# Kernel optimization log

Hardware: AMD Instinct MI355X
Metric: run time of the kernel (lower is better)

The kernel has to match this reference:

```python
import jax, jax.numpy as jnp
import numpy as np

B, L, DM = 4, 2048, 1024  # batch, seq len (== l_max, global kernel), d_model; head_dim = 1


def setup_inputs() -> dict:
    key = jax.random.key(0)
    ks = jax.random.split(key, 13)
    n = lambda k, shape, s=1.0: jax.random.normal(k, shape, dtype=jnp.float32) * s
    W_SCALE = 0.02   # keeps activations well-conditioned through the chained convs
    K_SCALE = 0.02
    return {
        "u": n(ks[0], (B, L, DM)),
        "Wq": n(ks[1], (DM, DM), W_SCALE), "bq": n(ks[2], (DM,), W_SCALE),
        "Wk": n(ks[3], (DM, DM), W_SCALE), "bk": n(ks[4], (DM,), W_SCALE),
        "Wv": n(ks[5], (DM, DM), W_SCALE), "bv": n(ks[6], (DM,), W_SCALE),
        "k_kernel": n(ks[7], (DM, L), K_SCALE),
        "k_D": n(ks[8], (DM,)),
        "ssm_kernel": n(ks[9], (DM, L), K_SCALE),
        "D": n(ks[10], (DM,)),
        "Wo": n(ks[11], (DM, DM), W_SCALE), "bo": n(ks[12], (DM,), W_SCALE),
    }


def reference(u, Wq, bq, Wk, bk, Wv, bv, k_kernel, k_D, ssm_kernel, D, Wo, bo):
    # u: (B, L, H) with H = d_model (head_dim = 1)
    Lseq = u.shape[1]
    fft_size = 2 * Lseq  # zero-pad to 2L for linear (causal) convolution

    # q/k/v projections -> (B, H, L)
    q = jnp.einsum('blh,dh->bdl', u, Wq) + bq[None, :, None]
    k = jnp.einsum('blh,dh->bdl', u, Wk) + bk[None, :, None]
    v = jnp.einsum('blh,dh->bdl', u, Wv) + bv[None, :, None]

    # shift conv on k: k <- k_kernel * k (causal FFT conv) + k_D * k
    k_kernel_f = jnp.fft.rfft(k_kernel, n=fft_size)           # (H, F)
    k_f = jnp.fft.rfft(k, n=fft_size)                          # (B, H, F)
    shift_k = jnp.fft.irfft(k_kernel_f[None] * k_f, n=fft_size)[..., :Lseq]
    k = shift_k + k_D[None, :, None] * k

    # head_dim == 1: kv outer product collapses to elementwise gate
    kv = k * v                                                 # (B, H, L)

    # ssm conv on kv (torch's 1/fft_size + norm='forward' irfft == standard irfft)
    kv_f = jnp.fft.rfft(kv, n=fft_size)                        # (B, H, F)
    ssm_kernel_f = jnp.fft.rfft(ssm_kernel, n=fft_size)        # (H, F)
    y = jnp.fft.irfft(kv_f * ssm_kernel_f[None], n=fft_size)[..., :Lseq]
    y = y + kv * D[None, :, None]                              # D skip

    # q gating, then output projection
    y = y * q                                                  # (B, H, L)
    y = jnp.swapaxes(y, 1, 2)                                  # (B, L, H)
    return jnp.einsum('blh,oh->blo', y, Wo) + bo
```

## Files before the change

kernel.cpp:

```cpp
#include <hip/hip_runtime.h>
#include <hip/hip_bf16.h>
#include <stdint.h>

#define DM   1024
#define LSEQ 2048
#define NB   4

typedef __attribute__((ext_vector_type(8))) short  short8;
typedef __attribute__((ext_vector_type(4))) float  floatx4;

__device__ __forceinline__ ushort f2b(float x) {
    union { float f; uint32_t u; } v; v.f = x;
    uint32_t b = v.u + 0x7FFF + ((v.u >> 16) & 1);
    return (ushort)(b >> 16);
}
__device__ __forceinline__ float b2f(ushort x) {
    union { uint32_t u; float f; } v; v.u = ((uint32_t)x) << 16;
    return v.f;
}

__global__ __launch_bounds__(256) void cvt_all_kernel(const float* __restrict__ u,
                                                      const float* __restrict__ Wq,
                                                      const float* __restrict__ Wk,
                                                      const float* __restrict__ Wv,
                                                      const float* __restrict__ Wo,
                                                      ushort* __restrict__ U16,
                                                      ushort* __restrict__ Wcat) {
    const int nu  = NB * LSEQ * DM / 8;
    const int per = DM * DM / 8;
    int i = blockIdx.x * 256 + threadIdx.x;
    const float* src; ushort* dst; int j;
    if (i < nu) { src = u; dst = U16; j = i; }
    else {
        int k = i - nu;
        int r = k / per;
        src = (r == 0) ? Wq : (r == 1) ? Wk : (r == 2) ? Wv : Wo;
        dst = Wcat + (size_t)r * (DM * DM);
        j = k - r * per;
    }
    const float4* p = (const float4*)src + (size_t)j * 2;
    float4 a = p[0], b = p[1];
    union { ushort us[8]; uint4 v; } o;
    o.us[0] = f2b(a.x); o.us[1] = f2b(a.y); o.us[2] = f2b(a.z); o.us[3] = f2b(a.w);
    o.us[4] = f2b(b.x); o.us[5] = f2b(b.y); o.us[6] = f2b(b.z); o.us[7] = f2b(b.w);
    *(uint4*)(dst + (size_t)j * 8) = o.v;
}

template <int MODE>
__global__ __launch_bounds__(512, 2) void gemm_8p(const ushort* __restrict__ Aw,
                                                  const ushort* __restrict__ Bw,
                                                  const float* __restrict__ b0,
                                                  const float* __restrict__ b1,
                                                  const float* __restrict__ b2,
                                                  void* __restrict__ C0v,
                                                  void* __restrict__ C1v,
                                                  void* __restrict__ C2v,
                                                  int N, int nbx) {
    constexpr int K = 1024, BK = 64, NT = K / BK;
    __shared__ char lds[131072];

    const int tid   = threadIdx.x;
    const int wave  = tid >> 6;
    const int lane  = tid & 63;
    const int qlane = lane & 15;
    const int qk    = lane >> 4;
    const int z7    = qlane & 7;
    const int wm    = wave >> 2;
    const int wn    = wave & 3;

    int flat = blockIdx.y * nbx + blockIdx.x;
    int nwg  = nbx * gridDim.y;
    int swz  = (flat & 7) * (nwg >> 3) + (flat >> 3);
    const int tn = (swz % nbx) * 256;
    const int tm = (swz / nbx) * 256;

    const int srcChunkOff   = (((lane & 7) ^ (lane >> 3)) * 8);
    const int srcRowInSlice = (lane >> 3);

#define STAGE_H(TT, ISB, H)                                                                   \
    {                                                                                         \
        const ushort* gbase = (ISB) ? Bw : Aw;                                                \
        const int trow = ((ISB) ? tn : tm) + (H) * 128 + wave * 16 + srcRowInSlice;           \
        char* dst = lds + ((ISB) ? 65536 : 0) + ((((TT) & 1) * 2 + (H)) * 16384) + wave * 2048; \
        const int k0_ = (TT) * BK;                                                            \
        _Pragma("unroll")                                                                     \
        for (int j = 0; j < 2; ++j) {                                                         \
            const ushort* src = gbase + (size_t)(trow + j * 8) * K + k0_ + srcChunkOff;       \
            __builtin_amdgcn_global_load_lds(                                                 \
                (const __attribute__((address_space(1))) void*)src,                           \
                (__attribute__((address_space(3))) void*)(dst + j * 1024), 16, 0, 0);         \
        }                                                                                     \
    }

    short8 af[4][2], af2[4][2], bf0[2][2], bf1[2][2];
    floatx4 acc[2][2][4][2] = {};

#define LDA(TT, MH, AF)                                                                       \
    {                                                                                         \
        const char* Ab = lds + ((((TT) & 1) * 2 + (MH)) * 16384);                             \
        _Pragma("unroll")                                                                     \
        for (int i = 0; i < 4; ++i) {                                                         \
            int lr = wm * 64 + i * 16 + qlane;                                                \
            _Pragma("unroll")                                                                 \
            for (int ks = 0; ks < 2; ++ks)                                                    \
                AF[i][ks] = *(const short8*)(Ab + lr * 128 + (((ks * 4 + qk) ^ z7) << 4));    \
        }                                                                                     \
    }
#define LDB(TT, NH, BF)                                                                       \
    {                                                                                         \
        const char* Bb = lds + 65536 + ((((TT) & 1) * 2 + (NH)) * 16384);                     \
        _Pragma("unroll")                                                                     \
        for (int j = 0; j < 2; ++j) {                                                         \
            int lr = wn * 32 + j * 16 + qlane;                                                \
            _Pragma("unroll")                                                                 \
            for (int ks = 0; ks < 2; ++ks)                                                    \
                BF[j][ks] = *(const short8*)(Bb + lr * 128 + (((ks * 4 + qk) ^ z7) << 4));    \
        }                                                                                     \
    }
#define MFMAQ(MH, NH, AF, BF)                                                                 \
    __builtin_amdgcn_s_setprio(1);                                                           \
    _Pragma("unroll")                                                                         \
    for (int ks = 0; ks < 2; ++ks)                                                            \
        _Pragma("unroll")                                                                     \
        for (int i = 0; i < 4; ++i)                                                           \
            _Pragma("unroll")                                                                 \
            for (int j = 0; j < 2; ++j)                                                       \
                acc[MH][NH][i][j] = __builtin_amdgcn_mfma_f32_16x16x32_bf16(                  \
                    AF[i][ks], BF[j][ks], acc[MH][NH][i][j], 0, 0, 0);                        \
    __builtin_amdgcn_s_setprio(0);
#define BARX  __builtin_amdgcn_s_barrier(); __builtin_amdgcn_sched_barrier(0)

    STAGE_H(0, 0, 0); STAGE_H(0, 1, 0); STAGE_H(0, 1, 1); STAGE_H(0, 0, 1);
    STAGE_H(1, 0, 0); STAGE_H(1, 1, 0); STAGE_H(1, 1, 1);
    asm volatile("s_waitcnt vmcnt(6)" ::: "memory");
    BARX;
    LDA(0, 0, af); LDB(0, 0, bf0);

    for (int t = 0; t < NT; ++t) {
        if (t + 1 < NT) STAGE_H(t + 1, 0, 1);
        LDB(t, 1, bf1);
        MFMAQ(0, 0, af, bf0);
        BARX;
        if (t + 2 < NT) STAGE_H(t + 2, 0, 0);
        LDA(t, 1, af2);
        MFMAQ(0, 1, af, bf1);
        BARX;
        if (t + 2 < NT) STAGE_H(t + 2, 1, 0);
        MFMAQ(1, 0, af2, bf0);
        BARX;
        if (t + 2 < NT) STAGE_H(t + 2, 1, 1);
        if (t + 2 < NT)      { asm volatile("s_waitcnt vmcnt(6)" ::: "memory"); }
        else if (t + 1 < NT) { asm volatile("s_waitcnt vmcnt(0)" ::: "memory"); }
        BARX;
        if (t + 1 < NT) { LDA(t + 1, 0, af); LDB(t + 1, 0, bf0); }
        MFMAQ(1, 1, af2, bf1);
    }
#undef STAGE_H
#undef LDA
#undef LDB
#undef MFMAQ
#undef BARX

#pragma unroll
    for (int mh = 0; mh < 2; ++mh)
#pragma unroll
    for (int nh = 0; nh < 2; ++nh)
#pragma unroll
    for (int i = 0; i < 4; ++i)
#pragma unroll
    for (int j = 0; j < 2; ++j) {
        int n  = tn + nh * 128 + wn * 32 + j * 16 + qlane;
        int m0 = tm + mh * 128 + wm * 64 + i * 16 + qk * 4;
        if (MODE == 0) {
            int proj = n >> 10, dd = n & (DM - 1);
            const float* bb = (proj == 0) ? b0 : (proj == 1) ? b1 : b2;
            ushort* Cb      = (ushort*)((proj == 0) ? C0v : (proj == 1) ? C1v : C2v);
            float bv = bb[dd];
            int b = m0 >> 11, l = m0 & (LSEQ - 1);
            ushort4 val;
            val.x = f2b(acc[mh][nh][i][j][0] + bv);
            val.y = f2b(acc[mh][nh][i][j][1] + bv);
            val.z = f2b(acc[mh][nh][i][j][2] + bv);
            val.w = f2b(acc[mh][nh][i][j][3] + bv);
            *(ushort4*)(Cb + ((size_t)b * DM + dd) * LSEQ + l) = val;
        } else {
            float* C0 = (float*)C0v;
            float bv = b0[n];
#pragma unroll
            for (int r = 0; r < 4; ++r)
                C0[(size_t)(m0 + r) * N + n] = acc[mh][nh][i][j][r] + bv;
        }
    }
}

template <int MODE>
__global__ __launch_bounds__(512, 2) void gemm_bt2(const ushort* __restrict__ Aw,
                                                   const ushort* __restrict__ Bw,
                                                   const float* __restrict__ b0,
                                                   const float* __restrict__ b1,
                                                   const float* __restrict__ b2,
                                                   void* __restrict__ C0v,
                                                   void* __restrict__ C1v,
                                                   void* __restrict__ C2v,
                                                   int M, int N, int K, int nbx) {
    constexpr int BM = 128, BN = 256, BK = 64;
    constexpr int BUFB = 49152;
    __shared__ char lds[3 * BUFB];

    const int tid   = threadIdx.x;
    const int wave  = tid >> 6;
    const int lane  = tid & 63;
    const int qlane = lane & 15;
    const int qk    = lane >> 4;

    int flat = blockIdx.y * nbx + blockIdx.x;
    int nwg  = nbx * gridDim.y;
    int swz  = (flat & 7) * (nwg >> 3) + (flat >> 3);
    const int tn = (swz % nbx) * BN;
    const int tm = (swz / nbx) * BM;

    const int wmo = (wave >> 2) * 64;
    const int wno = (wave & 3) * 64;
    const int NT  = K / BK;

#define STAGE(kt, p)                                                                          \
    {                                                                                         \
        const int k0_ = (kt) * BK;                                                            \
        char* Ab_ = lds + (p) * BUFB;                                                         \
        char* Bb_ = Ab_ + 16384;                                                              \
        _Pragma("unroll")                                                                     \
        for (int j = 0; j < 2; ++j) {                                                         \
            int id = wave * 64 + lane + j * 512;                                              \
            int row = id >> 3, s = id & 7;                                                    \
            const ushort* src = Aw + (size_t)(tm + row) * K + k0_ + ((s ^ (row & 7)) * 8);    \
            __builtin_amdgcn_global_load_lds((const __attribute__((address_space(1))) void*)src, \
                (__attribute__((address_space(3))) void*)(Ab_ + wave * 1024 + j * 8192), 16, 0, 0); \
        }                                                                                     \
        _Pragma("unroll")                                                                     \
        for (int j = 0; j < 4; ++j) {                                                         \
            int id = wave * 64 + lane + j * 512;                                              \
            int row = id >> 3, s = id & 7;                                                    \
            const ushort* src = Bw + (size_t)(tn + row) * K + k0_ + ((s ^ (row & 7)) * 8);    \
            __builtin_amdgcn_global_load_lds((const __attribute__((address_space(1))) void*)src, \
                (__attribute__((address_space(3))) void*)(Bb_ + wave * 1024 + j * 8192), 16, 0, 0); \
        }                                                                                     \
    }

    floatx4 acc[4][4] = {};

    STAGE(0, 0);
    STAGE(1, 1);

    const int z7 = qlane & 7;

    for (int t = 0; t < NT; ++t) {
        const int cur = t % 3;
        if (t < NT - 1) asm volatile("s_waitcnt vmcnt(6)" ::: "memory");
        else            asm volatile("s_waitcnt vmcnt(0)" ::: "memory");
        __builtin_amdgcn_s_barrier();
        __builtin_amdgcn_sched_barrier(0);

        if (t + 2 < NT) STAGE(t + 2, (t + 2) % 3);

        const char* Ab = lds + cur * BUFB;
        const char* Bb = Ab + 16384;
#pragma unroll
        for (int kk = 0; kk < 2; ++kk) {
            const int slot = ((kk * 4 + qk) ^ z7) << 4;
            short8 af[4], bfv[4];
#pragma unroll
            for (int i = 0; i < 4; ++i) {
                int r = wmo + i * 16 + qlane;
                af[i] = *(const short8*)(Ab + r * 128 + slot);
            }
#pragma unroll
            for (int j = 0; j < 4; ++j) {
                int r = wno + j * 16 + qlane;
                bfv[j] = *(const short8*)(Bb + r * 128 + slot);
            }
            __builtin_amdgcn_s_setprio(1);
#pragma unroll
            for (int i = 0; i < 4; ++i)
#pragma unroll
                for (int j = 0; j < 4; ++j)
                    acc[i][j] = __builtin_amdgcn_mfma_f32_16x16x32_bf16(af[i], bfv[j], acc[i][j], 0, 0, 0);
            __builtin_amdgcn_s_setprio(0);
        }
    }
#undef STAGE

#pragma unroll
    for (int i = 0; i < 4; ++i) {
#pragma unroll
        for (int j = 0; j < 4; ++j) {
            int n  = tn + wno + j * 16 + qlane;
            int m0 = tm + wmo + i * 16 + qk * 4;
            if (MODE == 0) {
                int proj = n >> 10, dd = n & (DM - 1);
                const float* bb = (proj == 0) ? b0 : (proj == 1) ? b1 : b2;
                ushort* Cb      = (ushort*)((proj == 0) ? C0v : (proj == 1) ? C1v : C2v);
                float bv = bb[dd];
                int b = m0 >> 11, l = m0 & (LSEQ - 1);
                ushort4 val;
                val.x = f2b(acc[i][j][0] + bv);
                val.y = f2b(acc[i][j][1] + bv);
                val.z = f2b(acc[i][j][2] + bv);
                val.w = f2b(acc[i][j][3] + bv);
                *(ushort4*)(Cb + ((size_t)b * DM + dd) * LSEQ + l) = val;
            } else {
                float* C0 = (float*)C0v;
                float bv = b0[n];
#pragma unroll
                for (int r = 0; r < 4; ++r)
                    C0[(size_t)(m0 + r) * N + n] = acc[i][j][r] + bv;
            }
        }
    }
}

#define KSTR 2096
#define XSTR 2248

__global__ __launch_bounds__(512) void conv_fused_kernel(const ushort* __restrict__ x,
                                                         const float* __restrict__ ker1,
                                                         const float* __restrict__ scale1,
                                                         const ushort* __restrict__ gate1,
                                                         const float* __restrict__ ker2,
                                                         const float* __restrict__ scale2,
                                                         const ushort* __restrict__ gate2,
                                                         ushort* __restrict__ out) {
    __shared__ ushort krev1[KSTR];
    __shared__ ushort krev2[KSTR];
    __shared__ ushort xs[4 * XSTR];
    const int d    = blockIdx.x;
    const int tid  = threadIdx.x;
    const int wave = tid >> 6;
    const int lane = tid & 63;

    {
        int b = wave >> 1, half = wave & 1;
        const ushort* src = x + ((size_t)b * DM + d) * LSEQ + half * 1024 + lane * 8;
        char* dst = (char*)xs + b * (XSTR * 2) + 256 + half * 2048;
#pragma unroll
        for (int c = 0; c < 2; ++c)
            __builtin_amdgcn_global_load_lds((const __attribute__((address_space(1))) void*)(src + c * 512),
                                             (__attribute__((address_space(3))) void*)(dst + c * 1024),
                                             16, 0, 0);
    }
    {
        int e0 = tid * 4;
        float4 k1 = *(const float4*)(ker1 + (size_t)d * LSEQ + e0);
        float4 k2 = *(const float4*)(ker2 + (size_t)d * LSEQ + e0);
        ushort4 o1, o2;
        o1.x = f2b(k1.w); o1.y = f2b(k1.z); o1.z = f2b(k1.y); o1.w = f2b(k1.x);
        o2.x = f2b(k2.w); o2.y = f2b(k2.z); o2.z = f2b(k2.y); o2.w = f2b(k2.x);
        *(ushort4*)(krev1 + (2060 - e0)) = o1;
        *(ushort4*)(krev2 + (2060 - e0)) = o2;
        uint4 z = {0, 0, 0, 0};
        if (tid < 2) {
            *(uint4*)((char*)krev1 + tid * 16) = z;
            *(uint4*)((char*)krev2 + tid * 16) = z;
        }
        if (tid >= 2 && tid < 6) {
            *(uint4*)((char*)krev1 + 4128 + (tid - 2) * 16) = z;
            *(uint4*)((char*)krev2 + 4128 + (tid - 2) * 16) = z;
        }
        if (tid >= 64 && tid < 128) {
            int b = (tid - 64) >> 4, c = (tid - 64) & 15;
            *(uint4*)((char*)xs + b * (XSTR * 2) + c * 16) = z;
        }
        if (tid >= 128 && tid < 144) {
            int b = (tid - 128) >> 2, c = (tid - 128) & 3;
            *(uint4*)((char*)xs + b * (XSTR * 2) + 4352 + c * 16) = z;
        }
    }
    __syncthreads();

    const int qn = lane & 15;
    const int qk = lane >> 4;

    int g[2] = {wave, 15 - wave};
    const int smax_all = 128 * (15 - wave) + 128;

    const int lbase = (qn & 3) * XSTR + 128 + 16 * (qn >> 2) + 8 * qk;

#define CSTEP(KR, ACC, SS, FP)                                                               \
    {                                                                                        \
        int b_el = 2063 - qn + 8 * qk - (SS);                                                \
        int A0 = b_el & ~3;                                                                  \
        uint2 w0 = *(const uint2*)((KR) + A0);                                               \
        uint2 w1 = *(const uint2*)((KR) + A0 + 4);                                           \
        uint2 w2 = *(const uint2*)((KR) + A0 + 8);                                           \
        int qsel = (b_el >> 1) & 1;                                                          \
        uint sh  = (uint)(b_el & 1) * 16u;                                                   \
        uint e0 = qsel ? w0.y : w0.x;                                                        \
        uint e1 = qsel ? w1.x : w0.y;                                                        \
        uint e2 = qsel ? w1.y : w1.x;                                                        \
        uint e3 = qsel ? w2.x : w1.y;                                                        \
        uint e4 = qsel ? w2.y : w2.x;                                                        \
        union { uint u[4]; short8 v; } Af;                                                   \
        Af.u[0] = __builtin_amdgcn_alignbit(e1, e0, sh);                                     \
        Af.u[1] = __builtin_amdgcn_alignbit(e2, e1, sh);                                     \
        Af.u[2] = __builtin_amdgcn_alignbit(e3, e2, sh);                                     \
        Af.u[3] = __builtin_amdgcn_alignbit(e4, e3, sh);                                     \
        _Pragma("unroll")                                                                    \
        for (int gi = 0; gi < 2; ++gi) {                                                     \
            if ((SS) <= 128 * g[gi] + 128) {                                                 \
                short8 fN = *(const short8*)(xs + lbase + 128 * g[gi] - (SS));               \
                ACC[gi][0] = __builtin_amdgcn_mfma_f32_16x16x32_bf16(Af.v, fN, ACC[gi][0], 0, 0, 0); \
                ACC[gi][1] = __builtin_amdgcn_mfma_f32_16x16x32_bf16(Af.v, FP[gi], ACC[gi][1], 0, 0, 0); \
                FP[gi] = fN;                                                                 \
            }                                                                                \
        }                                                                                    \
    }

    {
        floatx4 acc[2][2] = {};
        short8 fE[2], fO[2];
#pragma unroll
        for (int gi = 0; gi < 2; ++gi) {
            fE[gi] = *(const short8*)(xs + lbase + 128 * g[gi] + 64);
            fO[gi] = *(const short8*)(xs + lbase + 128 * g[gi] + 32);
        }
        for (int s = 0; s <= smax_all; s += 64) {
            CSTEP(krev1, acc, s, fE);
            if (s + 32 <= smax_all) CSTEP(krev1, acc, s + 32, fO);
        }

        __syncthreads();
        const float sc = scale1[d];
#pragma unroll
        for (int gi = 0; gi < 2; ++gi) {
#pragma unroll
            for (int m = 0; m < 2; ++m) {
                int p  = 8 * g[gi] + 4 * m + (qn >> 2);
                int b  = qn & 3;
                int l0 = 16 * p + 4 * qk;
                size_t off = ((size_t)b * DM + d) * LSEQ + l0;
                ushort4 xv = *(const ushort4*)(xs + b * XSTR + 128 + l0);
                ushort4 gv = *(const ushort4*)(gate1 + off);
                ushort4 ov;
                ov.x = f2b((acc[gi][m][0] + sc * b2f(xv.x)) * b2f(gv.x));
                ov.y = f2b((acc[gi][m][1] + sc * b2f(xv.y)) * b2f(gv.y));
                ov.z = f2b((acc[gi][m][2] + sc * b2f(xv.z)) * b2f(gv.z));
                ov.w = f2b((acc[gi][m][3] + sc * b2f(xv.w)) * b2f(gv.w));
                *(ushort4*)(xs + b * XSTR + 128 + l0) = ov;
            }
        }
        __syncthreads();
    }

    {
        floatx4 acc[2][2] = {};
        short8 fE[2], fO[2];
#pragma unroll
        for (int gi = 0; gi < 2; ++gi) {
            fE[gi] = *(const short8*)(xs + lbase + 128 * g[gi] + 64);
            fO[gi] = *(const short8*)(xs + lbase + 128 * g[gi] + 32);
        }
        for (int s = 0; s <= smax_all; s += 64) {
            CSTEP(krev2, acc, s, fE);
            if (s + 32 <= smax_all) CSTEP(krev2, acc, s + 32, fO);
        }

        const float sc = scale2[d];
#pragma unroll
        for (int gi = 0; gi < 2; ++gi) {
#pragma unroll
            for (int m = 0; m < 2; ++m) {
                int p  = 8 * g[gi] + 4 * m + (qn >> 2);
                int b  = qn & 3;
                int l0 = 16 * p + 4 * qk;
                size_t off = ((size_t)b * DM + d) * LSEQ + l0;
                ushort4 xv = *(const ushort4*)(xs + b * XSTR + 128 + l0);
                ushort4 gv = *(const ushort4*)(gate2 + off);
                ushort4 ov;
                ov.x = f2b((acc[gi][m][0] + sc * b2f(xv.x)) * b2f(gv.x));
                ov.y = f2b((acc[gi][m][1] + sc * b2f(xv.y)) * b2f(gv.y));
                ov.z = f2b((acc[gi][m][2] + sc * b2f(xv.z)) * b2f(gv.z));
                ov.w = f2b((acc[gi][m][3] + sc * b2f(xv.w)) * b2f(gv.w));
                *(ushort4*)(out + off) = ov;
            }
        }
    }
#undef CSTEP
}

__global__ __launch_bounds__(256) void transpose_bf16(const ushort* __restrict__ in,
                                                      ushort* __restrict__ out) {
    __shared__ ushort t[32][36];
    const int l0 = blockIdx.x * 32;
    const int d0 = blockIdx.y * 32;
    const int b  = blockIdx.z;
    const int q  = threadIdx.x & 7;
    const int r  = threadIdx.x >> 3;
    *(ushort4*)(&t[r][q * 4]) = *(const ushort4*)(in + ((size_t)b * DM + d0 + r) * LSEQ + l0 + q * 4);
    __syncthreads();
    ushort4 o;
    o.x = t[q * 4 + 0][r]; o.y = t[q * 4 + 1][r]; o.z = t[q * 4 + 2][r]; o.w = t[q * 4 + 3][r];
    *(ushort4*)(out + ((size_t)b * LSEQ + l0 + r) * DM + d0 + q * 4) = o;
}

extern "C" void kernel_launch(void* const* d_in, const int* in_sizes, int n_in,
                              void* d_out, int out_size, void* d_ws, size_t ws_size,
                              hipStream_t stream) {
    const float* u        = (const float*)d_in[0];
    const float* Wq       = (const float*)d_in[1];
    const float* bq       = (const float*)d_in[2];
    const float* Wk       = (const float*)d_in[3];
    const float* bk       = (const float*)d_in[4];
    const float* Wv       = (const float*)d_in[5];
    const float* bv       = (const float*)d_in[6];
    const float* k_kernel = (const float*)d_in[7];
    const float* k_D      = (const float*)d_in[8];
    const float* ssm_ker  = (const float*)d_in[9];
    const float* Dv       = (const float*)d_in[10];
    const float* Wo       = (const float*)d_in[11];
    const float* bo       = (const float*)d_in[12];
    float* outp = (float*)d_out;

    char* ws = (char*)d_ws;
    ushort* Q    = (ushort*)(ws);
    ushort* KV   = (ushort*)(ws + (16ull << 20));
    ushort* V    = (ushort*)(ws + (32ull << 20));
    ushort* U16  = (ushort*)(ws + (48ull << 20));
    ushort* YT   = (ushort*)(ws + (64ull << 20));
    ushort* Wcat = (ushort*)(ws + (80ull << 20));

    const int nu = NB * LSEQ * DM / 8, nw = 4 * DM * DM / 8;
    cvt_all_kernel<<<(nu + nw) / 256, 256, 0, stream>>>(u, Wq, Wk, Wv, Wo, U16, Wcat);

    dim3 g1(3 * DM / 256, NB * LSEQ / 256);
    gemm_8p<0><<<g1, 512, 0, stream>>>(U16, Wcat, bq, bk, bv, Q, KV, V,
                                       3 * DM, 3 * DM / 256);

    conv_fused_kernel<<<DM, 512, 0, stream>>>(KV, k_kernel, k_D, V, ssm_ker, Dv, Q, KV);

    dim3 g2(LSEQ / 32, DM / 32, NB);
    transpose_bf16<<<g2, 256, 0, stream>>>(KV, YT);

    dim3 g3(DM / 256, NB * LSEQ / 128);
    gemm_bt2<1><<<g3, 512, 0, stream>>>(YT, Wcat + 3 * DM * DM, bo, bo, bo,
                                        outp, outp, outp, NB * LSEQ, DM, DM, DM / 256);
}
```

Measured before the change: 162.6 us.

## Unify GEMMs into templated 128xBN ping-pong kernel with 384-wide QKV tiles

Replaces the 256x256 QKV GEMM and the separate triple-buffered output GEMM with one templated kernel using 128-row tiles and a configurable N width (384 for QKV, 256 for output). The pipeline stages whole A/B k-tiles two steps ahead with double buffering and alternates A fragment registers across unrolled tile pairs. The QKV grid changes from 12x32 to 8x64 workgroups, which alters wave balance across CUs and per-tile reuse. The output GEMM loses its three-stage buffer in favour of two stages. A leftover dead STAGE_B macro definition is left in the source.

```diff
diff --git a/kernel.cpp b/kernel.cpp
--- a/kernel.cpp
+++ b/kernel.cpp
@@ -46,8 +46,8 @@
     *(uint4*)(dst + (size_t)j * 8) = o.v;
 }
 
-template <int MODE>
-__global__ __launch_bounds__(512, 2) void gemm_8p(const ushort* __restrict__ Aw,
+template <int MODE, int BN>
+__global__ __launch_bounds__(512, 2) void gemm_v2(const ushort* __restrict__ Aw,
                                                   const ushort* __restrict__ Bw,
                                                   const float* __restrict__ b0,
                                                   const float* __restrict__ b1,
@@ -57,7 +57,12 @@
                                                   void* __restrict__ C2v,
                                                   int N, int nbx) {
     constexpr int K = 1024, BK = 64, NT = K / BK;
-    __shared__ char lds[131072];
+    constexpr int BM     = 128;
+    constexpr int NJH    = BN / 128;
+    constexpr int ASLOT  = BM * 128;
+    constexpr int BSLOT  = BN * 128;
+    constexpr int BOFF   = 2 * ASLOT;
+    __shared__ char lds[BOFF + 2 * BSLOT];
 
     const int tid   = threadIdx.x;
     const int wave  = tid >> 6;
@@ -71,33 +76,59 @@
     int flat = blockIdx.y * nbx + blockIdx.x;
     int nwg  = nbx * gridDim.y;
     int swz  = (flat & 7) * (nwg >> 3) + (flat >> 3);
-    const int tn = (swz % nbx) * 256;
-    const int tm = (swz / nbx) * 256;
-
-    const int srcChunkOff   = (((lane & 7) ^ (lane >> 3)) * 8);
-    const int srcRowInSlice = (lane >> 3);
-
-#define STAGE_H(TT, ISB, H)                                                                   \
-    {                                                                                         \
-        const ushort* gbase = (ISB) ? Bw : Aw;                                                \
-        const int trow = ((ISB) ? tn : tm) + (H) * 128 + wave * 16 + srcRowInSlice;           \
-        char* dst = lds + ((ISB) ? 65536 : 0) + ((((TT) & 1) * 2 + (H)) * 16384) + wave * 2048; \
+    const int tn = (swz % nbx) * BN;
+    const int tm = (swz / nbx) * BM;
+
+    const int srcChunkOff = ((lane & 7) ^ (lane >> 3)) * 8;
+    const int srcRow      = lane >> 3;
+
+#define STAGE_A(TT)                                                                           \
+    {                                                                                         \
+        const int trow = tm + wave * 16 + srcRow;                                             \
+        char* dst = lds + ((TT) & 1) * ASLOT + wave * 2048;                                   \
         const int k0_ = (TT) * BK;                                                            \
         _Pragma("unroll")                                                                     \
         for (int j = 0; j < 2; ++j) {                                                         \
-            const ushort* src = gbase + (size_t)(trow + j * 8) * K + k0_ + srcChunkOff;       \
+            const ushort* src = Aw + (size_t)(trow + j * 8) * K + k0_ + srcChunkOff;          \
             __builtin_amdgcn_global_load_lds(                                                 \
                 (const __attribute__((address_space(1))) void*)src,                           \
                 (__attribute__((address_space(3))) void*)(dst + j * 1024), 16, 0, 0);         \
         }                                                                                     \
     }
-
-    short8 af[4][2], af2[4][2], bf0[2][2], bf1[2][2];
-    floatx4 acc[2][2][4][2] = {};
-
-#define LDA(TT, MH, AF)                                                                       \
-    {                                                                                         \
-        const char* Ab = lds + ((((TT) & 1) * 2 + (MH)) * 16384);                             \
+#define STAGE_B(TT, H)                                                                        \
+    {                                                                                         \
+        const int rbase = (H) * (BN / 2) + wave * (8 * NJH);                                  \
+        const int trow  = tn + rbase + srcRow;                                                \
+        char* dst = lds + BOFF + ((TT) & 1) * BSLOT + rbase * 128;                            \
+        const int k0_ = (TT) * BK;                                                            \
+        _Pragma("unroll")                                                                     \
+        for (int j = 0; j < NJH; ++j) {                                                       \
+            const ushort* src = Bw + (size_t)(trow + j * 8) * K + k0_ + srcChunkOff;          \
+            __builtin_amdgcn_global_lds(0);                                                   \
+        }                                                                                     \
+    }
+#undef STAGE_B
+#define STAGE_B(TT, H)                                                                        \
+    {                                                                                         \
+        const int rbase = (H) * (BN / 2) + wave * (8 * NJH);                                  \
+        const int trow  = tn + rbase + srcRow;                                                \
+        char* dst = lds + BOFF + ((TT) & 1) * BSLOT + rbase * 128;                            \
+        const int k0_ = (TT) * BK;                                                            \
+        _Pragma("unroll")                                                                     \
+        for (int j = 0; j < NJH; ++j) {                                                       \
+            const ushort* src = Bw + (size_t)(trow + j * 8) * K + k0_ + srcChunkOff;          \
+            __builtin_amdgcn_global_load_lds(                                                 \
+                (const __attribute__((address_space(1))) void*)src,                           \
+                (__attribute__((address_space(3))) void*)(dst + j * 1024), 16, 0, 0);         \
+        }                                                                                     \
+    }
+
+    short8 afA[4][2], afB[4][2], bf0[NJH][2], bf1[NJH][2];
+    floatx4 acc[2][4][NJH] = {};
+
+#define LDA(TT, AF)                                                                           \
+    {                                                                                         \
+        const char* Ab = lds + ((TT) & 1) * ASLOT;                                            \
         _Pragma("unroll")                                                                     \
         for (int i = 0; i < 4; ++i) {                                                         \
             int lr = wm * 64 + i * 16 + qlane;                                                \
@@ -108,69 +139,74 @@
     }
 #define LDB(TT, NH, BF)                                                                       \
     {                                                                                         \
-        const char* Bb = lds + 65536 + ((((TT) & 1) * 2 + (NH)) * 16384);                     \
-        _Pragma("unroll")                                                                     \
-        for (int j = 0; j < 2; ++j) {                                                         \
-            int lr = wn * 32 + j * 16 + qlane;                                                \
+        const char* Bb = lds + BOFF + ((TT) & 1) * BSLOT;                                     \
+        _Pragma("unroll")                                                                     \
+        for (int j = 0; j < NJH; ++j) {                                                       \
+            int lr = wn * (BN / 4) + (NH) * (NJH * 16) + j * 16 + qlane;                      \
             _Pragma("unroll")                                                                 \
             for (int ks = 0; ks < 2; ++ks)                                                    \
                 BF[j][ks] = *(const short8*)(Bb + lr * 128 + (((ks * 4 + qk) ^ z7) << 4));    \
         }                                                                                     \
     }
-#define MFMAQ(MH, NH, AF, BF)                                                                 \
+#define MFMAQ(NH, AF, BF)                                                                     \
     __builtin_amdgcn_s_setprio(1);                                                           \
     _Pragma("unroll")                                                                         \
     for (int ks = 0; ks < 2; ++ks)                                                            \
         _Pragma("unroll")                                                                     \
         for (int i = 0; i < 4; ++i)                                                           \
             _Pragma("unroll")                                                                 \
-            for (int j = 0; j < 2; ++j)                                                       \
-                acc[MH][NH][i][j] = __builtin_amdgcn_mfma_f32_16x16x32_bf16(                  \
-                    AF[i][ks], BF[j][ks], acc[MH][NH][i][j], 0, 0, 0);                        \
+            for (int j = 0; j < NJH; ++j)                                                     \
+                acc[NH][i][j] = __builtin_amdgcn_mfma_f32_16x16x32_bf16(                      \
+                    AF[i][ks], BF[j][ks], acc[NH][i][j], 0, 0, 0);                            \
     __builtin_amdgcn_s_setprio(0);
 #define BARX  __builtin_amdgcn_s_barrier(); __builtin_amdgcn_sched_barrier(0)
-
-    STAGE_H(0, 0, 0); STAGE_H(0, 1, 0); STAGE_H(0, 1, 1); STAGE_H(0, 0, 1);
-    STAGE_H(1, 0, 0); STAGE_H(1, 1, 0); STAGE_H(1, 1, 1);
-    asm volatile("s_waitcnt vmcnt(6)" ::: "memory");
+#define VM_STEADY                                                                             \
+    do { if constexpr (BN == 384) asm volatile("s_waitcnt vmcnt(8)" ::: "memory");            \
+         else                     asm volatile("s_waitcnt vmcnt(6)" ::: "memory"); } while (0)
+
+    STAGE_A(0); STAGE_B(0, 0); STAGE_B(0, 1);
+    STAGE_A(1); STAGE_B(1, 0); STAGE_B(1, 1);
+    VM_STEADY;
     BARX;
-    LDA(0, 0, af); LDB(0, 0, bf0);
-
-    for (int t = 0; t < NT; ++t) {
-        if (t + 1 < NT) STAGE_H(t + 1, 0, 1);
-        LDB(t, 1, bf1);
-        MFMAQ(0, 0, af, bf0);
-        BARX;
-        if (t + 2 < NT) STAGE_H(t + 2, 0, 0);
-        LDA(t, 1, af2);
-        MFMAQ(0, 1, af, bf1);
-        BARX;
-        if (t + 2 < NT) STAGE_H(t + 2, 1, 0);
-        MFMAQ(1, 0, af2, bf0);
-        BARX;
-        if (t + 2 < NT) STAGE_H(t + 2, 1, 1);
-        if (t + 2 < NT)      { asm volatile("s_waitcnt vmcnt(6)" ::: "memory"); }
-        else if (t + 1 < NT) { asm volatile("s_waitcnt vmcnt(0)" ::: "memory"); }
-        BARX;
-        if (t + 1 < NT) { LDA(t + 1, 0, af); LDB(t + 1, 0, bf0); }
-        MFMAQ(1, 1, af2, bf1);
-    }
-#undef STAGE_H
+    LDA(0, afA); LDB(0, 0, bf0);
+    asm volatile("s_waitcnt lgkmcnt(0)" ::: "memory");
+    __builtin_amdgcn_sched_barrier(0);
+    BARX;
+
+#define TILE(T, AFc, AFn)                                                                     \
+    {                                                                                         \
+        LDB(T, 1, bf1);                                                                       \
+        MFMAQ(0, AFc, bf0);                                                                   \
+        BARX;                                                                                 \
+        if ((T) + 2 < NT) { STAGE_A((T) + 2); STAGE_B((T) + 2, 0); STAGE_B((T) + 2, 1); }     \
+        MFMAQ(1, AFc, bf1);                                                                   \
+        if ((T) + 2 < NT)      { VM_STEADY; }                                                 \
+        else if ((T) + 1 < NT) { asm volatile("s_waitcnt vmcnt(0)" ::: "memory"); }           \
+        BARX;                                                                                 \
+        if ((T) + 1 < NT) { LDA((T) + 1, AFn); LDB((T) + 1, 0, bf0); }                        \
+    }
+
+    for (int t = 0; t < NT; t += 2) {
+        TILE(t,     afA, afB);
+        TILE(t + 1, afB, afA);
+    }
+#undef TILE
+#undef STAGE_A
+#undef STAGE_B
 #undef LDA
 #undef LDB
 #undef MFMAQ
 #undef BARX
-
-#pragma unroll
-    for (int mh = 0; mh < 2; ++mh)
+#undef VM_STEADY
+
 #pragma unroll
     for (int nh = 0; nh < 2; ++nh)
 #pragma unroll
     for (int i = 0; i < 4; ++i)
 #pragma unroll
-    for (int j = 0; j < 2; ++j) {
-        int n  = tn + nh * 128 + wn * 32 + j * 16 + qlane;
-        int m0 = tm + mh * 128 + wm * 64 + i * 16 + qk * 4;
+    for (int j = 0; j < NJH; ++j) {
+        int n  = tn + wn * (BN / 4) + nh * (NJH * 16) + j * 16 + qlane;
+        int m0 = tm + wm * 64 + i * 16 + qk * 4;
         if (MODE == 0) {
             int proj = n >> 10, dd = n & (DM - 1);
             const float* bb = (proj == 0) ? b0 : (proj == 1) ? b1 : b2;
@@ -178,142 +214,17 @@
             float bv = bb[dd];
             int b = m0 >> 11, l = m0 & (LSEQ - 1);
             ushort4 val;
-            val.x = f2b(acc[mh][nh][i][j][0] + bv);
-            val.y = f2b(acc[mh][nh][i][j][1] + bv);
-            val.z = f2b(acc[mh][nh][i][j][2] + bv);
-            val.w = f2b(acc[mh][nh][i][j][3] + bv);
+            val.x = f2b(acc[nh][i][j][0] + bv);
+            val.y = f2b(acc[nh][i][j][1] + bv);
+            val.z = f2b(acc[nh][i][j][2] + bv);
+            val.w = f2b(acc[nh][i][j][3] + bv);
             *(ushort4*)(Cb + ((size_t)b * DM + dd) * LSEQ + l) = val;
         } else {
             float* C0 = (float*)C0v;
             float bv = b0[n];
 #pragma unroll
             for (int r = 0; r < 4; ++r)
-                C0[(size_t)(m0 + r) * N + n] = acc[mh][nh][i][j][r] + bv;
-        }
-    }
-}
-
-template <int MODE>
-__global__ __launch_bounds__(512, 2) void gemm_bt2(const ushort* __restrict__ Aw,
-                                                   const ushort* __restrict__ Bw,
-                                                   const float* __restrict__ b0,
-                                                   const float* __restrict__ b1,
-                                                   const float* __restrict__ b2,
-                                                   void* __restrict__ C0v,
-                                                   void* __restrict__ C1v,
-                                                   void* __restrict__ C2v,
-                                                   int M, int N, int K, int nbx) {
-    constexpr int BM = 128, BN = 256, BK = 64;
-    constexpr int BUFB = 49152;
-    __shared__ char lds[3 * BUFB];
-
-    const int tid   = threadIdx.x;
-    const int wave  = tid >> 6;
-    const int lane  = tid & 63;
-    const int qlane = lane & 15;
-    const int qk    = lane >> 4;
-
-    int flat = blockIdx.y * nbx + blockIdx.x;
-    int nwg  = nbx * gridDim.y;
-    int swz  = (flat & 7) * (nwg >> 3) + (flat >> 3);
-    const int tn = (swz % nbx) * BN;
-    const int tm = (swz / nbx) * BM;
-
-    const int wmo = (wave >> 2) * 64;
-    const int wno = (wave & 3) * 64;
-    const int NT  = K / BK;
-
-#define STAGE(kt, p)                                                                          \
-    {                                                                                         \
-        const int k0_ = (kt) * BK;                                                            \
-        char* Ab_ = lds + (p) * BUFB;                                                         \
-        char* Bb_ = Ab_ + 16384;                                                              \
-        _Pragma("unroll")                                                                     \
-        for (int j = 0; j < 2; ++j) {                                                         \
-            int id = wave * 64 + lane + j * 512;                                              \
-            int row = id >> 3, s = id & 7;                                                    \
-            const ushort* src = Aw + (size_t)(tm + row) * K + k0_ + ((s ^ (row & 7)) * 8);    \
-            __builtin_amdgcn_global_load_lds((const __attribute__((address_space(1))) void*)src, \
-                (__attribute__((address_space(3))) void*)(Ab_ + wave * 1024 + j * 8192), 16, 0, 0); \
-        }                                                                                     \
-        _Pragma("unroll")                                                                     \
-        for (int j = 0; j < 4; ++j) {                                                         \
-            int id = wave * 64 + lane + j * 512;                                              \
-            int row = id >> 3, s = id & 7;                                                    \
-            const ushort* src = Bw + (size_t)(tn + row) * K + k0_ + ((s ^ (row & 7)) * 8);    \
-            __builtin_amdgcn_global_load_lds((const __attribute__((address_space(1))) void*)src, \
-                (__attribute__((address_space(3))) void*)(Bb_ + wave * 1024 + j * 8192), 16, 0, 0); \
-        }                                                                                     \
-    }
-
-    floatx4 acc[4][4] = {};
-
-    STAGE(0, 0);
-    STAGE(1, 1);
-
-    const int z7 = qlane & 7;
-
-    for (int t = 0; t < NT; ++t) {
-        const int cur = t % 3;
-        if (t < NT - 1) asm volatile("s_waitcnt vmcnt(6)" ::: "memory");
-        else            asm volatile("s_waitcnt vmcnt(0)" ::: "memory");
-        __builtin_amdgcn_s_barrier();
-        __builtin_amdgcn_sched_barrier(0);
-
-        if (t + 2 < NT) STAGE(t + 2, (t + 2) % 3);
-
-        const char* Ab = lds + cur * BUFB;
-        const char* Bb = Ab + 16384;
-#pragma unroll
-        for (int kk = 0; kk < 2; ++kk) {
-            const int slot = ((kk * 4 + qk) ^ z7) << 4;
-            short8 af[4], bfv[4];
-#pragma unroll
-            for (int i = 0; i < 4; ++i) {
-                int r = wmo + i * 16 + qlane;
-                af[i] = *(const short8*)(Ab + r * 128 + slot);
-            }
-#pragma unroll
-            for (int j = 0; j < 4; ++j) {
-                int r = wno + j * 16 + qlane;
-                bfv[j] = *(const short8*)(Bb + r * 128 + slot);
-            }
-            __builtin_amdgcn_s_setprio(1);
-#pragma unroll
-            for (int i = 0; i < 4; ++i)
-#pragma unroll
-                for (int j = 0; j < 4; ++j)
-                    acc[i][j] = __builtin_amdgcn_mfma_f32_16x16x32_bf16(af[i], bfv[j], acc[i][j], 0, 0, 0);
-            __builtin_amdgcn_s_setprio(0);
-        }
-    }
-#undef STAGE
-
-#pragma unroll
-    for (int i = 0; i < 4; ++i) {
-#pragma unroll
-        for (int j = 0; j < 4; ++j) {
-            int n  = tn + wno + j * 16 + qlane;
-            int m0 = tm + wmo + i * 16 + qk * 4;
-            if (MODE == 0) {
-                int proj = n >> 10, dd = n & (DM - 1);
-                const float* bb = (proj == 0) ? b0 : (proj == 1) ? b1 : b2;
-                ushort* Cb      = (ushort*)((proj == 0) ? C0v : (proj == 1) ? C1v : C2v);
-                float bv = bb[dd];
-                int b = m0 >> 11, l = m0 & (LSEQ - 1);
-                ushort4 val;
-                val.x = f2b(acc[i][j][0] + bv);
-                val.y = f2b(acc[i][j][1] + bv);
-                val.z = f2b(acc[i][j][2] + bv);
-                val.w = f2b(acc[i][j][3] + bv);
-                *(ushort4*)(Cb + ((size_t)b * DM + dd) * LSEQ + l) = val;
-            } else {
-                float* C0 = (float*)C0v;
-                float bv = b0[n];
-#pragma unroll
-                for (int r = 0; r < 4; ++r)
-                    C0[(size_t)(m0 + r) * N + n] = acc[i][j][r] + bv;
-            }
+                C0[(size_t)(m0 + r) * N + n] = acc[nh][i][j][r] + bv;
         }
     }
 }
@@ -530,9 +441,9 @@
     const int nu = NB * LSEQ * DM / 8, nw = 4 * DM * DM / 8;
     cvt_all_kernel<<<(nu + nw) / 256, 256, 0, stream>>>(u, Wq, Wk, Wv, Wo, U16, Wcat);
 
-    dim3 g1(3 * DM / 256, NB * LSEQ / 256);
-    gemm_8p<0><<<g1, 512, 0, stream>>>(U16, Wcat, bq, bk, bv, Q, KV, V,
-                                       3 * DM, 3 * DM / 256);
+    dim3 g1(3 * DM / 384, NB * LSEQ / 128);
+    gemm_v2<0, 384><<<g1, 512, 0, stream>>>(U16, Wcat, bq, bk, bv, Q, KV, V,
+                                            3 * DM, 3 * DM / 384);
 
     conv_fused_kernel<<<DM, 512, 0, stream>>>(KV, k_kernel, k_D, V, ssm_ker, Dv, Q, KV);
 
@@ -540,6 +451,6 @@
     transpose_bf16<<<g2, 256, 0, stream>>>(KV, YT);
 
     dim3 g3(DM / 256, NB * LSEQ / 128);
-    gemm_bt2<1><<<g3, 512, 0, stream>>>(YT, Wcat + 3 * DM * DM, bo, bo, bo,
-                                        outp, outp, outp, NB * LSEQ, DM, DM, DM / 256);
-}
+    gemm_v2<1, 256><<<g3, 512, 0, stream>>>(YT, Wcat + 3 * DM * DM, bo, bo, bo,
+                                            outp, outp, outp, DM, DM / 256);
+}
```

Measured after the change: 160.0 us. About the same (-1.6%).
